# Kernel tuning notes

Measured on AMD Instinct MI355X. Metric: run time of the kernel, lower is better.

## Reference

```python
import jax, jax.numpy as jnp
import numpy as np

S, I, IN_DIM, PROJ_DIM, OUT_DIM = 128, 384, 256, 32, 128
LN_EPS = 1e-5


def _layer_norm(x):
    # utils.normalize in OmegaFold: F.layer_norm over last dim, no affine params
    mu = jnp.mean(x, axis=-1, keepdims=True)
    var = jnp.var(x, axis=-1, keepdims=True)
    return (x - mu) * jax.lax.rsqrt(var + LN_EPS)


def setup_inputs() -> dict:
    key = jax.random.key(0)
    k0, k1, k2, k3 = jax.random.split(key, 4)
    node_repr = jax.random.normal(k0, (S, I, IN_DIM), dtype=jnp.float32)
    mask = (jax.random.uniform(k1, (S, I)) < 0.9).astype(jnp.float32)
    W_proj = jax.random.normal(k2, (IN_DIM, 2 * PROJ_DIM), dtype=jnp.float32) / np.sqrt(IN_DIM)
    b_proj = jnp.zeros((2 * PROJ_DIM,), dtype=jnp.float32)
    out_weights = jax.random.normal(k3, (PROJ_DIM, PROJ_DIM, OUT_DIM), dtype=jnp.float32) * 0.02
    out_bias = jnp.zeros((OUT_DIM,), dtype=jnp.float32)
    return {
        "node_repr": node_repr,
        "mask": mask,
        "W_proj": W_proj,
        "b_proj": b_proj,
        "out_weights": out_weights,
        "out_bias": out_bias,
    }


def reference(node_repr, mask, W_proj, b_proj, out_weights, out_bias):
    # LayerNorm (no affine) -> linear projection to 2*proj_dim
    x = _layer_norm(node_repr)                       # [s, i, in_dim]
    act = x @ W_proj + b_proj                        # [s, i, 2d]
    m = mask[..., None]                              # [s, i, 1]
    act = act * m
    # mask-pair counts: einsum('si,sj->ij')
    norm = jnp.einsum("si,sj->ij", mask, mask)[..., None]  # [i, j, 1]
    l = act[..., :PROJ_DIM]                          # [s, i, d]
    r = act[..., PROJ_DIM:]                          # [s, j, e]
    # outer-product mean over s, then contract (d,e)->f with the 3-tensor
    outer = jnp.einsum("sid,sje->ijde", l, r)        # [i, j, d, e]
    out = jnp.einsum("ijde,def->ijf", outer, out_weights) + out_bias  # [i, j, f]
    return out / (norm + 0.001)
```

## Files before the change

kernel.cpp:

```cpp
#include <hip/hip_runtime.h>

#define S_DIM 128
#define I_DIM 384
#define IN_DIM 256
#define PD 32
#define ODIM 128

typedef __attribute__((ext_vector_type(8))) __bf16 bf16x8;
typedef __attribute__((ext_vector_type(4))) float f32x4;

#define MFMA16(a, b, c) __builtin_amdgcn_mfma_f32_16x16x32_bf16((a), (b), (c), 0, 0, 0)

__device__ inline unsigned short f2bf(float f) {
    unsigned int u = __builtin_bit_cast(unsigned int, f);
    unsigned int r = (u + 0x7FFFu + ((u >> 16) & 1u)) >> 16;
    return (unsigned short)r;
}

__global__ void prep_cast(const float* __restrict__ Wp, const float* __restrict__ W2,
                          unsigned short* __restrict__ WpT, unsigned short* __restrict__ W2t) {
    int t = blockIdx.x * 256 + threadIdx.x;
    if (t < 64 * 256) {
        int f = t >> 8, k = t & 255;
        WpT[t] = f2bf(Wp[k * 64 + f]);
    }
    if (t < 128 * 1024) {
        int f = t >> 10, de = t & 1023;
        int e = de >> 5, d = de & 31;
        W2t[t] = f2bf(W2[(d * 32 + e) * 128 + f]);
    }
}

__global__ void norm_kernel(const float* __restrict__ mask, float* __restrict__ invn) {
    __shared__ float mi[S_DIM][16];
    __shared__ float mj[S_DIM][16];
    int t = threadIdx.x;
    int i0 = blockIdx.y * 16, j0 = blockIdx.x * 16;
    for (int p = 0; p < 8; ++p) {
        int s = p * 16 + (t >> 4);
        int c = t & 15;
        mi[s][c] = mask[s * I_DIM + i0 + c];
        mj[s][c] = mask[s * I_DIM + j0 + c];
    }
    __syncthreads();
    int ii = t >> 4, jj = t & 15;
    float acc = 0.f;
#pragma unroll 8
    for (int s = 0; s < S_DIM; ++s) acc += mi[s][ii] * mj[s][jj];
    invn[(i0 + ii) * I_DIM + (j0 + jj)] = 1.0f / (acc + 0.001f);
}

__global__ __launch_bounds__(256, 4) void ln_proj(const float* __restrict__ x,
                                                  const float* __restrict__ mask,
                                                  const float* __restrict__ bias,
                                                  const unsigned short* __restrict__ WpT_g,
                                                  unsigned short* __restrict__ lT,
                                                  unsigned short* __restrict__ rT) {
    __shared__ unsigned short xsh[64 * 264];
    int t = threadIdx.x;
    int w = t >> 6, lane = t & 63;
    int i = blockIdx.x >> 1;
    int s0 = (blockIdx.x & 1) * 64;

    float4 vbuf[4];
#pragma unroll
    for (int p = 0; p < 4; ++p)
        vbuf[p] = *(const float4*)(x + ((size_t)(s0 + w * 16 + p) * I_DIM + i) * IN_DIM + lane * 4);

    for (int it = 0; it < 16; ++it) {
        float4 v = vbuf[it & 3];
        if (it + 4 < 16)
            vbuf[it & 3] = *(const float4*)(x + ((size_t)(s0 + w * 16 + it + 4) * I_DIM + i) * IN_DIM + lane * 4);
        float s1 = v.x + v.y + v.z + v.w;
        float s2 = v.x * v.x + v.y * v.y + v.z * v.z + v.w * v.w;
#pragma unroll
        for (int off = 32; off >= 1; off >>= 1) {
            s1 += __shfl_xor(s1, off);
            s2 += __shfl_xor(s2, off);
        }
        float mu = s1 * (1.f / 256.f);
        float var = s2 * (1.f / 256.f) - mu * mu;
        float rs = rsqrtf(var + 1e-5f);
        unsigned int h0 = f2bf((v.x - mu) * rs);
        unsigned int h1 = f2bf((v.y - mu) * rs);
        unsigned int h2 = f2bf((v.z - mu) * rs);
        unsigned int h3 = f2bf((v.w - mu) * rs);
        uint2 pk;
        pk.x = h0 | (h1 << 16);
        pk.y = h2 | (h3 << 16);
        *(uint2*)&xsh[(w * 16 + it) * 264 + lane * 4] = pk;
    }
    __syncthreads();

    int l15 = lane & 15, q = lane >> 4;
    f32x4 acc[4];
#pragma unroll
    for (int nt = 0; nt < 4; ++nt) acc[nt] = (f32x4){0.f, 0.f, 0.f, 0.f};

    for (int k0 = 0; k0 < 256; k0 += 32) {
        bf16x8 a = *(bf16x8*)&xsh[(w * 16 + l15) * 264 + k0 + q * 8];
#pragma unroll
        for (int nt = 0; nt < 4; ++nt) {
            bf16x8 b = *(const bf16x8*)&WpT_g[(nt * 16 + l15) * 256 + k0 + q * 8];
            acc[nt] = MFMA16(a, b, acc[nt]);
        }
    }

    float mval[4];
#pragma unroll
    for (int reg = 0; reg < 4; ++reg)
        mval[reg] = mask[(size_t)(s0 + w * 16 + q * 4 + reg) * I_DIM + i];

    __syncthreads();
    unsigned short* trsh = xsh;

#pragma unroll
    for (int nt = 0; nt < 4; ++nt) {
        int f = nt * 16 + l15;
        float bv = bias[f];
        unsigned int lo = (unsigned int)f2bf((acc[nt][0] + bv) * mval[0]) |
                          ((unsigned int)f2bf((acc[nt][1] + bv) * mval[1]) << 16);
        unsigned int hi = (unsigned int)f2bf((acc[nt][2] + bv) * mval[2]) |
                          ((unsigned int)f2bf((acc[nt][3] + bv) * mval[3]) << 16);
        uint2 pk; pk.x = lo; pk.y = hi;
        *(uint2*)&trsh[f * 72 + w * 16 + q * 4] = pk;
    }
    __syncthreads();

    {
        int fr = t >> 2, so = (t & 3) * 16;
        unsigned short* dst = ((fr < 32) ? lT : rT) + ((size_t)(i * 32 + (fr & 31)) * 128 + s0 + so);
        *(uint4*)dst = *(uint4*)&trsh[fr * 72 + so];
        *(uint4*)(dst + 8) = *(uint4*)&trsh[fr * 72 + so + 8];
    }
}

__global__ __launch_bounds__(512, 4) void fused_kernel(const unsigned short* __restrict__ lT,
                                                       const unsigned short* __restrict__ rT,
                                                       const unsigned short* __restrict__ W2t,
                                                       const float* __restrict__ invn,
                                                       const float* __restrict__ out_bias,
                                                       float* __restrict__ out) {
    __shared__ unsigned short sh[32768];
    char* shb = (char*)sh;
    int t = threadIdx.x;
    int w = t >> 6, lane = t & 63, l15 = lane & 15, q = lane >> 4;
    int bx = blockIdx.x;
    int by = blockIdx.y;
    int wm = w >> 1, wn = w & 1;

    {
        int row = t >> 2, c0 = (t & 3) * 32;
        const unsigned short* rbase = rT + (size_t)(bx * 128 + row) * 128 + c0;
        uint4 v0 = ((const uint4*)rbase)[0];
        uint4 v1 = ((const uint4*)rbase)[1];
        uint4 v2 = ((const uint4*)rbase)[2];
        uint4 v3 = ((const uint4*)rbase)[3];
        *(uint4*)&sh[row * 136 + c0] = v0;
        *(uint4*)&sh[row * 136 + c0 + 8] = v1;
        *(uint4*)&sh[row * 136 + c0 + 16] = v2;
        *(uint4*)&sh[row * 136 + c0 + 24] = v3;
    }

    const unsigned short* lbase = lT + (size_t)(by * 256 + wm * 64 + l15) * 128 + q * 8;
    bf16x8 a0_ = *(const bf16x8*)(lbase);
    bf16x8 a1_ = *(const bf16x8*)(lbase + 2048);
    bf16x8 a2_ = *(const bf16x8*)(lbase + 4096);
    bf16x8 a3_ = *(const bf16x8*)(lbase + 6144);
    __syncthreads();

    f32x4 acc[4][4];
#pragma unroll
    for (int mt = 0; mt < 4; ++mt)
#pragma unroll
        for (int nt = 0; nt < 4; ++nt) acc[mt][nt] = (f32x4){0.f, 0.f, 0.f, 0.f};

#pragma unroll
    for (int k0 = 0; k0 < 4; ++k0) {
        bf16x8 a[4];
        if (k0 == 0) {
            a[0] = a0_; a[1] = a1_; a[2] = a2_; a[3] = a3_;
        } else {
#pragma unroll
            for (int mt = 0; mt < 4; ++mt)
                a[mt] = *(const bf16x8*)(lbase + mt * 2048 + k0 * 32);
        }
#pragma unroll
        for (int nt = 0; nt < 4; ++nt) {
            bf16x8 b = *(bf16x8*)&sh[(wn * 64 + nt * 16 + l15) * 136 + k0 * 32 + q * 8];
#pragma unroll
            for (int mt = 0; mt < 4; ++mt)
                acc[mt][nt] = MFMA16(a[mt], b, acc[mt][nt]);
        }
    }
    __syncthreads();

#pragma unroll
    for (int mt = 0; mt < 4; ++mt) {
        int i_loc = wm * 2 + (mt >> 1);
        int dbase2 = ((mt & 1) * 16 + q * 4) * 2;
#pragma unroll
        for (int nt = 0; nt < 4; ++nt) {
            int pair = i_loc * 4 + wn * 2 + (nt >> 1);
            int e = (nt & 1) * 16 + l15;
            unsigned int lo = (unsigned int)f2bf(acc[mt][nt][0]) | ((unsigned int)f2bf(acc[mt][nt][1]) << 16);
            unsigned int hi = (unsigned int)f2bf(acc[mt][nt][2]) | ((unsigned int)f2bf(acc[mt][nt][3]) << 16);
            uint2 pk; pk.x = lo; pk.y = hi;
            *(uint2*)(shb + pair * 2048 + ((e * 64 + dbase2) ^ ((e & 7) << 4) ^ ((pair & 7) << 4))) = pk;
        }
    }

    const unsigned short* wrow = W2t + (size_t)(w * 16 + l15) * 1024 + q * 8;
    bf16x8 bp0 = *(const bf16x8*)(wrow);
    bf16x8 bp1 = *(const bf16x8*)(wrow + 32);
    bf16x8 bp2 = *(const bf16x8*)(wrow + 64);
    bf16x8 bp3 = *(const bf16x8*)(wrow + 96);
    __syncthreads();

    f32x4 acc3[2];
    acc3[0] = (f32x4){0.f, 0.f, 0.f, 0.f};
    acc3[1] = (f32x4){0.f, 0.f, 0.f, 0.f};
    char* gbase0 = shb + l15 * 2048;
    char* gbase1 = shb + (16 + l15) * 2048;
    int sx = (l15 & 7) << 4;

#pragma unroll
    for (int k0 = 0; k0 < 32; ++k0) {
        bf16x8 b;
        if (k0 == 0) b = bp0;
        else if (k0 == 1) b = bp1;
        else if (k0 == 2) b = bp2;
        else if (k0 == 3) b = bp3;
        else b = *(const bf16x8*)(wrow + k0 * 32);
        int off = ((k0 * 64 + q * 16) ^ ((k0 & 7) << 4)) ^ sx;
        bf16x8 a0 = *(bf16x8*)(gbase0 + off);
        bf16x8 a1 = *(bf16x8*)(gbase1 + off);
        acc3[0] = MFMA16(a0, b, acc3[0]);
        acc3[1] = MFMA16(a1, b, acc3[1]);
    }

    float bv = out_bias[w * 16 + l15];
#pragma unroll
    for (int mt3 = 0; mt3 < 2; ++mt3) {
#pragma unroll
        for (int reg = 0; reg < 4; ++reg) {
            int pair = mt3 * 16 + q * 4 + reg;
            int gi = by * 8 + (pair >> 2);
            int gj = bx * 4 + (pair & 3);
            float vinv = invn[gi * I_DIM + gj];
            out[((size_t)gi * I_DIM + gj) * 128 + w * 16 + l15] = (acc3[mt3][reg] + bv) * vinv;
        }
    }
}

extern "C" void kernel_launch(void* const* d_in, const int* in_sizes, int n_in,
                              void* d_out, int out_size, void* d_ws, size_t ws_size,
                              hipStream_t stream) {
    const float* node = (const float*)d_in[0];
    const float* mask = (const float*)d_in[1];
    const float* Wp   = (const float*)d_in[2];
    const float* bp   = (const float*)d_in[3];
    const float* W2   = (const float*)d_in[4];
    const float* bo   = (const float*)d_in[5];
    float* out = (float*)d_out;

    char* ws = (char*)d_ws;
    unsigned short* lT  = (unsigned short*)(ws);
    unsigned short* rT  = (unsigned short*)(ws + 3145728);
    unsigned short* W2t = (unsigned short*)(ws + 6291456);
    unsigned short* WpT = (unsigned short*)(ws + 6553600);
    float*          inv = (float*)(ws + 6586368);

    hipLaunchKernelGGL(prep_cast, dim3(512), dim3(256), 0, stream, Wp, W2, WpT, W2t);
    hipLaunchKernelGGL(norm_kernel, dim3(24, 24), dim3(256), 0, stream, mask, inv);
    hipLaunchKernelGGL(ln_proj, dim3(768), dim3(256), 0, stream, node, mask, bp, WpT, lT, rT);
    hipLaunchKernelGGL(fused_kernel, dim3(96, 48), dim3(512), 0, stream,
                       lT, rT, W2t, inv, bo, out);
}
```

Before: 335.3 us.

## Stream W2 slices into LDS via async global_load_lds double buffering

Reorders the bf16 W2 layout so each k-slice is contiguous, then uses global_load_lds DMA to prefetch W2 slices into a double-buffered shared-memory region during the second GEMM. Per-lane global loads inside the MFMA loop are replaced by LDS reads, with explicit waitcnt, sched barriers and setprio around the MFMAs. The aim is to hide W2 global latency behind compute. It adds 16KB of LDS per block and per-iteration synchronization that can stall the loop.

```diff
diff --git a/kernel.cpp b/kernel.cpp
--- a/kernel.cpp
+++ b/kernel.cpp
@@ -18,16 +18,17 @@
 }
 
 __global__ void prep_cast(const float* __restrict__ Wp, const float* __restrict__ W2,
-                          unsigned short* __restrict__ WpT, unsigned short* __restrict__ W2t) {
+                          unsigned short* __restrict__ WpT, unsigned short* __restrict__ W2s) {
     int t = blockIdx.x * 256 + threadIdx.x;
     if (t < 64 * 256) {
         int f = t >> 8, k = t & 255;
         WpT[t] = f2bf(Wp[k * 64 + f]);
     }
     if (t < 128 * 1024) {
-        int f = t >> 10, de = t & 1023;
-        int e = de >> 5, d = de & 31;
-        W2t[t] = f2bf(W2[(d * 32 + e) * 128 + f]);
+        int e = t >> 12;
+        int f = (t >> 5) & 127;
+        int d = t & 31;
+        W2s[t] = f2bf(W2[(d * 32 + e) * 128 + f]);
     }
 }
 
@@ -137,11 +138,12 @@
 
 __global__ __launch_bounds__(512, 4) void fused_kernel(const unsigned short* __restrict__ lT,
                                                        const unsigned short* __restrict__ rT,
-                                                       const unsigned short* __restrict__ W2t,
+                                                       const unsigned short* __restrict__ W2s,
                                                        const float* __restrict__ invn,
                                                        const float* __restrict__ out_bias,
                                                        float* __restrict__ out) {
     __shared__ unsigned short sh[32768];
+    __shared__ unsigned short w2b[8192];
     char* shb = (char*)sh;
     int t = threadIdx.x;
     int w = t >> 6, lane = t & 63, l15 = lane & 15, q = lane >> 4;
@@ -195,6 +197,15 @@
     }
     __syncthreads();
 
+#define DMA_W2(K0_)                                                                     \
+    __builtin_amdgcn_global_load_lds(                                                   \
+        (const __attribute__((address_space(1))) unsigned int*)(const void*)(W2s + (K0_) * 4096 + t * 8), \
+        (__attribute__((address_space(3))) unsigned int*)(void*)(&w2b[((K0_) & 1) * 4096 + w * 512]),     \
+        16, 0, 0)
+
+    DMA_W2(0);
+    DMA_W2(1);
+
 #pragma unroll
     for (int mt = 0; mt < 4; ++mt) {
         int i_loc = wm * 2 + (mt >> 1);
@@ -209,12 +220,6 @@
             *(uint2*)(shb + pair * 2048 + ((e * 64 + dbase2) ^ ((e & 7) << 4) ^ ((pair & 7) << 4))) = pk;
         }
     }
-
-    const unsigned short* wrow = W2t + (size_t)(w * 16 + l15) * 1024 + q * 8;
-    bf16x8 bp0 = *(const bf16x8*)(wrow);
-    bf16x8 bp1 = *(const bf16x8*)(wrow + 32);
-    bf16x8 bp2 = *(const bf16x8*)(wrow + 64);
-    bf16x8 bp3 = *(const bf16x8*)(wrow + 96);
     __syncthreads();
 
     f32x4 acc3[2];
@@ -223,21 +228,33 @@
     char* gbase0 = shb + l15 * 2048;
     char* gbase1 = shb + (16 + l15) * 2048;
     int sx = (l15 & 7) << 4;
-
-#pragma unroll
-    for (int k0 = 0; k0 < 32; ++k0) {
-        bf16x8 b;
-        if (k0 == 0) b = bp0;
-        else if (k0 == 1) b = bp1;
-        else if (k0 == 2) b = bp2;
-        else if (k0 == 3) b = bp3;
-        else b = *(const bf16x8*)(wrow + k0 * 32);
+    int brow = (w * 16 + l15) * 32 + q * 8;
+
+#pragma unroll 2
+    for (int k0 = 0; k0 < 31; ++k0) {
+        asm volatile("s_waitcnt vmcnt(1)" ::: "memory");
+        bf16x8 b = *(bf16x8*)&w2b[(k0 & 1) * 4096 + brow];
         int off = ((k0 * 64 + q * 16) ^ ((k0 & 7) << 4)) ^ sx;
+        bf16x8 a0 = *(bf16x8*)(gbase0 + off);
+        bf16x8 a1 = *(bf16x8*)(gbase1 + off);
+        asm volatile("s_waitcnt lgkmcnt(0)" ::: "memory");
+        if (k0 < 30) { DMA_W2(k0 + 2); }
+        __builtin_amdgcn_sched_barrier(0);
+        __builtin_amdgcn_s_setprio(1);
+        acc3[0] = MFMA16(a0, b, acc3[0]);
+        acc3[1] = MFMA16(a1, b, acc3[1]);
+        __builtin_amdgcn_s_setprio(0);
+    }
+    {
+        asm volatile("s_waitcnt vmcnt(0)" ::: "memory");
+        bf16x8 b = *(bf16x8*)&w2b[(31 & 1) * 4096 + brow];
+        int off = ((31 * 64 + q * 16) ^ ((31 & 7) << 4)) ^ sx;
         bf16x8 a0 = *(bf16x8*)(gbase0 + off);
         bf16x8 a1 = *(bf16x8*)(gbase1 + off);
         acc3[0] = MFMA16(a0, b, acc3[0]);
         acc3[1] = MFMA16(a1, b, acc3[1]);
     }
+#undef DMA_W2
 
     float bv = out_bias[w * 16 + l15];
 #pragma unroll
@@ -267,13 +284,13 @@
     char* ws = (char*)d_ws;
     unsigned short* lT  = (unsigned short*)(ws);
     unsigned short* rT  = (unsigned short*)(ws + 3145728);
-    unsigned short* W2t = (unsigned short*)(ws + 6291456);
+    unsigned short* W2s = (unsigned short*)(ws + 6291456);
     unsigned short* WpT = (unsigned short*)(ws + 6553600);
     float*          inv = (float*)(ws + 6586368);
 
-    hipLaunchKernelGGL(prep_cast, dim3(512), dim3(256), 0, stream, Wp, W2, WpT, W2t);
+    hipLaunchKernelGGL(prep_cast, dim3(512), dim3(256), 0, stream, Wp, W2, WpT, W2s);
     hipLaunchKernelGGL(norm_kernel, dim3(24, 24), dim3(256), 0, stream, mask, inv);
     hipLaunchKernelGGL(ln_proj, dim3(768), dim3(256), 0, stream, node, mask, bp, WpT, lT, rT);
     hipLaunchKernelGGL(fused_kernel, dim3(96, 48), dim3(512), 0, stream,
-                       lT, rT, W2t, inv, bo, out);
-}
+                       lT, rT, W2s, inv, bo, out);
+}
```

Result: faster. 269.3 us (-19.7%).
